# Kernel optimization log

Measured on AMD Instinct MI355X. Metric: run time of the kernel, lower is better.

Reference implementation:

```python
import jax, jax.numpy as jnp
import numpy as np

B, S, D, H, HD = 2, 4096, 768, 12, 64
W = 256           # one-sided window (attention_window=512)
C = S // W        # number of query chunks
NEG = -1e9


def _heads(x):
    # [B,S,D] -> [B,H,S,HD]
    return x.reshape(B, S, H, HD).transpose(0, 2, 1, 3)


def setup_inputs() -> dict:
    key = jax.random.key(0)
    ks = jax.random.split(key, 9)
    sc = 0.02
    w = lambda i: jax.random.normal(ks[i], (D, D), jnp.float32) * sc
    return {
        "hidden_states": jax.random.normal(ks[0], (B, S, D), jnp.float32),
        "Wq": w(1), "Wk": w(2), "Wv": w(3),
        "Wqg": w(4), "Wkg": w(5), "Wvg": w(6),
        "Wo": w(7),
        "attention_mask": jnp.ones((B, S), jnp.int32),
    }


def reference(hidden_states, Wq, Wk, Wv, Wqg, Wkg, Wvg, Wo, attention_mask):
    x = hidden_states
    scale = 1.0 / float(np.sqrt(HD))
    q = _heads(x @ Wq) * scale           # [B,H,S,HD]
    k = _heads(x @ Wk)
    v = _heads(x @ Wv)

    # ---- banded sliding-window attention (chunked, no [S,S] matrix) ----
    idx = jnp.arange(C)[:, None] * W + jnp.arange(3 * W)[None, :]   # [C,3W] into padded seq
    key_pos = idx - W                                               # absolute key position
    kp = jnp.pad(k, ((0, 0), (0, 0), (W, W), (0, 0)))
    vp = jnp.pad(v, ((0, 0), (0, 0), (W, W), (0, 0)))
    kc = kp[:, :, idx]                   # [B,H,C,3W,HD]
    vc = vp[:, :, idx]
    qc = q.reshape(B, H, C, W, HD)
    band = jnp.einsum('bhcqd,bhckd->bhcqk', qc, kc)  # [B,H,C,W,3W]

    qi = jnp.arange(W)[:, None]
    kj = jnp.arange(3 * W)[None, :]
    diag_ok = (kj >= qi) & (kj <= qi + 2 * W)              # |i-j| <= W
    valid = (key_pos >= 0) & (key_pos < S) & (key_pos != 0)  # in-range, dedupe global key 0
    mask = diag_ok[None, :, :] & valid[:, None, :]          # [C,W,3W]
    band = jnp.where(mask[None, None], band, NEG)

    # padding mask on keys
    m = jnp.where(attention_mask > 0, 0.0, NEG).astype(jnp.float32)  # [B,S]
    mp = jnp.pad(m, ((0, 0), (W, W)), constant_values=NEG)
    band = band + mp[:, idx][:, None, :, None, :]
    band = band.reshape(B, H, S, 3 * W)

    # every local query also attends to the global (CLS, pos 0) key
    gsc = jnp.einsum('bhsd,bhgd->bhsg', q, k[:, :, 0:1])   # [B,H,S,1]
    gsc = gsc + m[:, 0][:, None, None, None]

    scores = jnp.concatenate([gsc, band], axis=-1)          # [B,H,S,1+3W]
    probs = jax.nn.softmax(scores, axis=-1)
    pg = probs[..., :1]                                     # global-key prob
    pb = probs[..., 1:].reshape(B, H, C, W, 3 * W)
    out = jnp.einsum('bhcqk,bhckd->bhcqd', pb, vc).reshape(B, H, S, HD)
    out = out + pg * v[:, :, 0:1]

    # ---- global query (CLS) full attention with dedicated projections ----
    qg = _heads(x @ Wqg)[:, :, 0:1] * scale                 # [B,H,1,HD]
    kg = _heads(x @ Wkg)
    vg = _heads(x @ Wvg)
    gs = jnp.einsum('bhgd,bhsd->bhgs', qg, kg) + m[:, None, None, :]
    og = jnp.einsum('bhgs,bhsd->bhgd', jax.nn.softmax(gs, axis=-1), vg)
    out = out.at[:, :, 0:1].set(og)

    out = out.transpose(0, 2, 1, 3).reshape(B, S, D) @ Wo
    return out
```

## Files before the change

### kernel.cpp

```cpp
#include <hip/hip_runtime.h>

#define S_LEN 4096
#define NH 12
#define HDIM 64
#define DMODEL 768
#define NEGF -1.0e9f
#define TOK0_SPLITS 16

typedef __attribute__((ext_vector_type(8))) short bf16x8;
typedef __attribute__((ext_vector_type(4))) float f32x4;

__device__ __forceinline__ short f2b(float f) {
  union { float f; unsigned u; } v; v.f = f;
  unsigned r = v.u + 0x7fffu + ((v.u >> 16) & 1u);
  return (short)(r >> 16);
}
__device__ __forceinline__ float b2f(short s) {
  union { unsigned u; float f; } v; v.u = ((unsigned)(unsigned short)s) << 16;
  return v.f;
}

__global__ void k_conv_x(const float* __restrict__ x, short* __restrict__ xb, int n4) {
  int i = blockIdx.x * blockDim.x + threadIdx.x;
  if (i >= n4) return;
  float4 v = ((const float4*)x)[i];
  ((short4*)xb)[i] = make_short4(f2b(v.x), f2b(v.y), f2b(v.z), f2b(v.w));
}

__global__ void k_mv(const int* __restrict__ amask, float* __restrict__ mvb) {
  int b = blockIdx.y, s = blockIdx.x * 256 + threadIdx.x;
  mvb[b * S_LEN + s] = (s != 0 && amask[b * S_LEN + s] > 0) ? 0.f : NEGF;
}

__global__ void k_wt(const float* __restrict__ Wq, const float* __restrict__ Wk,
                     const float* __restrict__ Wv, const float* __restrict__ Wkg,
                     const float* __restrict__ Wvg, const float* __restrict__ Wo,
                     short* __restrict__ W5t, short* __restrict__ Wot) {
  __shared__ float tbuf[32][33];
  int z = blockIdx.z;
  const float* src; float scale = 1.f; short* dst;
  switch (z) {
    case 0: src = Wq;  scale = 0.125f * 1.44269504f; dst = W5t; break;
    case 1: src = Wk;  dst = W5t + 589824; break;
    case 2: src = Wv;  dst = W5t + 2 * 589824; break;
    case 3: src = Wkg; dst = W5t + 3 * 589824; break;
    case 4: src = Wvg; dst = W5t + 4 * 589824; break;
    default: src = Wo; dst = Wot; break;
  }
  int tx = threadIdx.x, ty = threadIdx.y;
  int kb = blockIdx.y * 32, nb = blockIdx.x * 32;
  for (int i = 0; i < 4; i++) tbuf[ty + 8 * i][tx] = src[(kb + ty + 8 * i) * 768 + nb + tx];
  __syncthreads();
  for (int i = 0; i < 4; i++)
    dst[(nb + ty + 8 * i) * 768 + kb + tx] = f2b(tbuf[tx][ty + 8 * i] * scale);
}

__global__ __launch_bounds__(256) void k_qg(const float* __restrict__ x,
                                            const float* __restrict__ Wqg,
                                            float* __restrict__ qg) {
  int h = blockIdx.x, b = blockIdx.y;
  int tid = threadIdx.x;
  int out = tid & 63, slice = tid >> 6;
  __shared__ float xr[768];
  __shared__ float ps[4][64];
  for (int i = tid; i < 768; i += 256) xr[i] = x[(long)b * S_LEN * 768 + i];
  __syncthreads();
  float a = 0.f;
  int n = h * 64 + out;
#pragma unroll 8
  for (int k = slice * 192; k < slice * 192 + 192; k++) a += xr[k] * Wqg[k * 768 + n];
  ps[slice][out] = a;
  __syncthreads();
  if (tid < 64)
    qg[b * 768 + h * 64 + tid] = (ps[0][tid] + ps[1][tid] + ps[2][tid] + ps[3][tid]) * 0.125f;
}

__global__ __launch_bounds__(256) void k_gemm(const short* __restrict__ A,
                                              const short* __restrict__ Bt, int K, int mode,
                                              short* __restrict__ qkv, float* __restrict__ outf) {
  __shared__ short Al[128 * 32];
  __shared__ short Bl[128 * 32];
  int bid = blockIdx.x;
  int xcd = bid & 7, ii = bid >> 3;
  int bm = xcd * 8 + (ii & 7), bn = ii >> 3;
  int tid = threadIdx.x;
  int bm0 = bm * 128, bn0 = bn * 128;
  int w = tid >> 6, lane = tid & 63, g = lane >> 4, r16 = lane & 15;
  int wr = (w >> 1) * 64, wc = (w & 1) * 64;
  f32x4 zero4 = {0.f, 0.f, 0.f, 0.f};
  f32x4 acc[4][4];
  for (int m = 0; m < 4; m++) for (int n = 0; n < 4; n++) acc[m][n] = zero4;
  int srow = w * 32 + (lane >> 2);
  int scol = (lane & 3) * 8;
  for (int kt = 0; kt < K; kt += 32) {
    for (int i = 0; i < 2; i++) {
      const short* ga = &A[(long)(bm0 + srow + i * 16) * K + kt + scol];
      const short* gb = &Bt[(long)(bn0 + srow + i * 16) * K + kt + scol];
      __builtin_amdgcn_global_load_lds(
          (const __attribute__((address_space(1))) void*)ga,
          (__attribute__((address_space(3))) void*)&Al[(w * 32 + i * 16) * 32], 16, 0, 0);
      __builtin_amdgcn_global_load_lds(
          (const __attribute__((address_space(1))) void*)gb,
          (__attribute__((address_space(3))) void*)&Bl[(w * 32 + i * 16) * 32], 16, 0, 0);
    }
    __syncthreads();
    bf16x8 af[4], bfv[4];
    for (int m = 0; m < 4; m++) af[m] = *(const bf16x8*)&Al[(wr + m * 16 + r16) * 32 + g * 8];
    for (int n = 0; n < 4; n++) bfv[n] = *(const bf16x8*)&Bl[(wc + n * 16 + r16) * 32 + g * 8];
    for (int m = 0; m < 4; m++)
      for (int n = 0; n < 4; n++)
        acc[m][n] = __builtin_amdgcn_mfma_f32_16x16x32_bf16(af[m], bfv[n], acc[m][n], 0, 0, 0);
    __syncthreads();
  }
  for (int m = 0; m < 4; m++)
    for (int n = 0; n < 4; n++)
      for (int reg = 0; reg < 4; reg++) {
        int row = bm0 + wr + m * 16 + g * 4 + reg;
        int col = bn0 + wc + n * 16 + r16;
        float val = acc[m][n][reg];
        if (mode == 0) {
          int proj = col / 768;
          int rem = col - proj * 768;
          int hh = rem >> 6, d = rem & 63;
          int bb = row >> 12, s = row & 4095;
          qkv[(long)proj * 6291456 + ((((long)bb * NH + hh) * S_LEN + s) << 6) + d] = f2b(val);
        } else {
          outf[(long)row * 768 + col] = val;
        }
      }
}

__global__ __launch_bounds__(256) void k_vt(const short* __restrict__ V, short* __restrict__ Vt) {
  __shared__ short buf[64][72];
  int st = blockIdx.x, bh = blockIdx.y;
  int tid = threadIdx.x;
  long base = (long)bh * S_LEN * HDIM;
  int s0 = st * 64;
  int r = tid >> 2, c = (tid & 3) * 16;
  *(int4*)&buf[r][c]     = *(const int4*)&V[base + (long)(s0 + r) * HDIM + c];
  *(int4*)&buf[r][c + 8] = *(const int4*)&V[base + (long)(s0 + r) * HDIM + c + 8];
  __syncthreads();
  int d = tid >> 2, sc = (tid & 3) * 16;
  short tmp[16];
#pragma unroll
  for (int j = 0; j < 16; j++) tmp[j] = buf[sc + j][d];
  long ob = base + (long)d * S_LEN + s0 + sc;
  *(int4*)&Vt[ob]     = *(const int4*)&tmp[0];
  *(int4*)&Vt[ob + 8] = *(const int4*)&tmp[8];
}

#define KVPAD 36
#define PSTRIDE 68

__device__ __forceinline__ void band_chunk(
    int ks0, int qrow0, int g, int r16,
    const bf16x8 (&qf)[2][2], const bf16x8 (&kf)[4][2], const bf16x8 (&vf)[4][2],
    const float (&mv)[4],
    float (&mstate)[2][4], float (&lstate)[2][4], f32x4 (&acc)[2][4],
    short* Plds) {
  int dlo = ks0 - qrow0;
  bool fullok = (dlo >= -224) && (dlo <= 192);
  for (int m = 0; m < 2; m++) {
    f32x4 s[4];
    f32x4 zero4 = {0.f, 0.f, 0.f, 0.f};
    for (int n = 0; n < 4; n++) {
      f32x4 z = __builtin_amdgcn_mfma_f32_16x16x32_bf16(qf[m][0], kf[n][0], zero4, 0, 0, 0);
      s[n] = __builtin_amdgcn_mfma_f32_16x16x32_bf16(qf[m][1], kf[n][1], z, 0, 0, 0);
    }
    float p[4][4], rmax[4];
    for (int reg = 0; reg < 4; reg++) rmax[reg] = NEGF;
    if (fullok) {
      for (int n = 0; n < 4; n++)
        for (int reg = 0; reg < 4; reg++) {
          float val = s[n][reg] + mv[n];
          p[n][reg] = val;
          rmax[reg] = fmaxf(rmax[reg], val);
        }
    } else {
      int qbase = qrow0 + m * 16 + g * 4;
      for (int n = 0; n < 4; n++) {
        int kpos = ks0 + n * 16 + r16;
        for (int reg = 0; reg < 4; reg++) {
          int qpos = qbase + reg;
          bool ok = (kpos >= qpos - 256) && (kpos <= qpos + 256);
          float val = ok ? (s[n][reg] + mv[n]) : NEGF;
          p[n][reg] = val;
          rmax[reg] = fmaxf(rmax[reg], val);
        }
      }
    }
    for (int reg = 0; reg < 4; reg++) {
      float r = rmax[reg];
      r = fmaxf(r, __shfl_xor(r, 1));
      r = fmaxf(r, __shfl_xor(r, 2));
      r = fmaxf(r, __shfl_xor(r, 4));
      r = fmaxf(r, __shfl_xor(r, 8));
      rmax[reg] = r;
    }
    bool over = false;
    for (int reg = 0; reg < 4; reg++) over = over || (rmax[reg] > mstate[m][reg] + 8.f);
    if (__any((int)over)) {
      float scal[4];
      for (int reg = 0; reg < 4; reg++) {
        float mn = fmaxf(mstate[m][reg], rmax[reg]);
        scal[reg] = __builtin_amdgcn_exp2f(mstate[m][reg] - mn);
        mstate[m][reg] = mn;
      }
      float rs[4] = {0.f, 0.f, 0.f, 0.f};
      for (int n = 0; n < 4; n++)
        for (int reg = 0; reg < 4; reg++) {
          float e = __builtin_amdgcn_exp2f(p[n][reg] - mstate[m][reg]);
          p[n][reg] = e;
          rs[reg] += e;
        }
      for (int reg = 0; reg < 4; reg++) {
        float r = rs[reg];
        r += __shfl_xor(r, 1);
        r += __shfl_xor(r, 2);
        r += __shfl_xor(r, 4);
        r += __shfl_xor(r, 8);
        lstate[m][reg] = lstate[m][reg] * scal[reg] + r;
      }
      for (int n = 0; n < 4; n++)
        for (int reg = 0; reg < 4; reg++) acc[m][n][reg] *= scal[reg];
    } else {
      float rs[4] = {0.f, 0.f, 0.f, 0.f};
      for (int n = 0; n < 4; n++)
        for (int reg = 0; reg < 4; reg++) {
          float e = __builtin_amdgcn_exp2f(p[n][reg] - mstate[m][reg]);
          p[n][reg] = e;
          rs[reg] += e;
        }
      for (int reg = 0; reg < 4; reg++) {
        float r = rs[reg];
        r += __shfl_xor(r, 1);
        r += __shfl_xor(r, 2);
        r += __shfl_xor(r, 4);
        r += __shfl_xor(r, 8);
        lstate[m][reg] += r;
      }
    }
    for (int n = 0; n < 4; n++)
      for (int reg = 0; reg < 4; reg++)
        Plds[(g * 4 + reg) * PSTRIDE + n * 16 + r16] = f2b(p[n][reg]);
    bf16x8 pa[2];
    for (int ks = 0; ks < 2; ks++)
      pa[ks] = *(const bf16x8*)&Plds[r16 * PSTRIDE + ks * 32 + g * 8];
    for (int n = 0; n < 4; n++)
      for (int ks = 0; ks < 2; ks++)
        acc[m][n] = __builtin_amdgcn_mfma_f32_16x16x32_bf16(pa[ks], vf[n][ks], acc[m][n], 0, 0, 0);
  }
}

__global__ __launch_bounds__(256, 2) void k_band(const short* __restrict__ Qb,
                                                 const short* __restrict__ Kb,
                                                 const short* __restrict__ Vb,
                                                 const short* __restrict__ Vtb,
                                                 const int* __restrict__ amask,
                                                 const float* __restrict__ mvb,
                                                 short* __restrict__ oattn) {
  int qtb = blockIdx.x, h = blockIdx.y, b = blockIdx.z;
  int tid = threadIdx.x, w = tid >> 6, lane = tid & 63, g = lane >> 4, r16 = lane & 15;
  long bhof = ((long)(b * NH + h)) * S_LEN * HDIM;
  __shared__ short Klds[2][2][64][KVPAD];
  __shared__ short Vlds[2][2][64][KVPAD];
  __shared__ short Plds[4][16 * PSTRIDE];
  int qb0 = qtb * 128;
  int qrow0 = qb0 + w * 32;

  bf16x8 qf[2][2];
  for (int m = 0; m < 2; m++)
    for (int ks = 0; ks < 2; ks++)
      qf[m][ks] = *(const bf16x8*)&Qb[bhof + (long)(qrow0 + m * 16 + r16) * HDIM + ks * 32 + g * 8];

  float mstate[2][4], lstate[2][4];
  f32x4 acc[2][4];
  {
    bf16x8 k0f[2];
    for (int ks = 0; ks < 2; ks++) k0f[ks] = *(const bf16x8*)&Kb[bhof + ks * 32 + g * 8];
    float part[2];
    for (int m = 0; m < 2; m++) {
      float p = 0.f;
      for (int ks = 0; ks < 2; ks++)
        for (int j = 0; j < 8; j++) p += b2f(qf[m][ks][j]) * b2f(k0f[ks][j]);
      p += __shfl_xor(p, 16);
      p += __shfl_xor(p, 32);
      part[m] = p;
    }
    float mask0 = (amask[b * S_LEN] > 0) ? 0.f : NEGF;
    float v0v[4];
    for (int n = 0; n < 4; n++) v0v[n] = b2f(Vb[bhof + n * 16 + r16]);
    for (int m = 0; m < 2; m++)
      for (int reg = 0; reg < 4; reg++) {
        mstate[m][reg] = __shfl(part[m], g * 4 + reg) + mask0;
        lstate[m][reg] = 1.f;
        for (int n = 0; n < 4; n++) acc[m][n][reg] = v0v[n];
      }
  }

  int c0 = (qb0 - 256) >> 6; if (c0 < 0) c0 = 0;
  int c1 = (qb0 + 127 + 256) >> 6; if (c1 > 63) c1 = 63;
  int wlo = (qrow0 - 256) >> 6;
  int whi = (qrow0 + 31 + 256) >> 6;

  int ss = tid >> 2, qq = tid & 3;
  int ksh = qq >> 1, qcol = (qq & 1) * 16;
  int4 rk0, rk1, rv0, rv1;
#define STAGE_LOAD(CI)                                                              \
  do {                                                                              \
    int _k = (CI) * 64;                                                             \
    const int4* gk = (const int4*)&Kb[bhof + (long)(_k + ss) * HDIM + qq * 16];     \
    rk0 = gk[0]; rk1 = gk[1];                                                       \
    const int4* gv = (const int4*)&Vtb[bhof + (long)ss * S_LEN + _k + qq * 16];     \
    rv0 = gv[0]; rv1 = gv[1];                                                       \
  } while (0)
#define STAGE_WRITE(BUF)                                                            \
  do {                                                                              \
    short* kd = &Klds[BUF][ksh][ss][qcol];                                          \
    *(int4*)kd = rk0; *(int4*)(kd + 8) = rk1;                                       \
    short* vd = &Vlds[BUF][ksh][ss][qcol];                                          \
    *(int4*)vd = rv0; *(int4*)(vd + 8) = rv1;                                       \
  } while (0)

  STAGE_LOAD(c0);
  STAGE_WRITE(0);
  __syncthreads();

  for (int ci = c0; ci <= c1; ci++) {
    int buf = (ci - c0) & 1;
    bool havenext = (ci + 1 <= c1);
    if (havenext) STAGE_LOAD(ci + 1);
    if (ci >= wlo && ci <= whi) {
      int ks0 = ci * 64;
      bf16x8 kf[4][2], vf[4][2];
      for (int n = 0; n < 4; n++)
        for (int ks = 0; ks < 2; ks++) {
          kf[n][ks] = *(const bf16x8*)&Klds[buf][ks][n * 16 + r16][g * 8];
          vf[n][ks] = *(const bf16x8*)&Vlds[buf][ks][n * 16 + r16][g * 8];
        }
      float mv[4];
      for (int n = 0; n < 4; n++) mv[n] = mvb[b * S_LEN + ks0 + n * 16 + r16];
      band_chunk(ks0, qrow0, g, r16, qf, kf, vf, mv, mstate, lstate, acc, &Plds[w][0]);
    }
    if (havenext) STAGE_WRITE(buf ^ 1);
    __syncthreads();
  }
#undef STAGE_LOAD
#undef STAGE_WRITE

  for (int m = 0; m < 2; m++)
    for (int n = 0; n < 4; n++)
      for (int reg = 0; reg < 4; reg++) {
        int token = qrow0 + m * 16 + g * 4 + reg;
        int col = h * 64 + n * 16 + r16;
        oattn[((long)b * S_LEN + token) * 768 + col] = f2b(acc[m][n][reg] / lstate[m][reg]);
      }
}

__global__ __launch_bounds__(256) void k_tok0_part(const float* __restrict__ qg,
                                                   const short* __restrict__ Kg,
                                                   const short* __restrict__ Vg,
                                                   const int* __restrict__ amask,
                                                   float* __restrict__ part) {
  int split = blockIdx.x, bhid = blockIdx.y;
  int b = bhid / NH, h = bhid % NH;
  long base = (long)bhid * S_LEN * HDIM;
  int tid = threadIdx.x, lane = tid & 63, w = tid >> 6;
  int s = split * 256 + tid;
  __shared__ float qgl[64];
  __shared__ float p_sh[256];
  __shared__ float red[4];
  __shared__ float psum[4][64];
  if (tid < 64) qgl[tid] = qg[b * 768 + h * 64 + tid];
  __syncthreads();
  float dot = 0.f;
  {
    const int4* kr = (const int4*)&Kg[base + (long)s * HDIM];
#pragma unroll
    for (int u = 0; u < 8; u++) {
      int4 pk = kr[u];
      const short* sp = (const short*)&pk;
      for (int j = 0; j < 8; j++) dot += qgl[u * 8 + j] * b2f(sp[j]);
    }
    dot += (amask[b * S_LEN + s] > 0) ? 0.f : NEGF;
  }
  float mx = dot;
  for (int o = 32; o; o >>= 1) mx = fmaxf(mx, __shfl_xor(mx, o));
  if (lane == 0) red[w] = mx;
  __syncthreads();
  mx = fmaxf(fmaxf(red[0], red[1]), fmaxf(red[2], red[3]));
  float e = __expf(dot - mx);
  p_sh[tid] = e;
  float sum = e;
  for (int o = 32; o; o >>= 1) sum += __shfl_xor(sum, o);
  __syncthreads();
  if (lane == 0) red[w] = sum;
  __syncthreads();
  sum = red[0] + red[1] + red[2] + red[3];
  int d = tid & 63, grp = tid >> 6;
  float a = 0.f;
  long vb = base + (long)(split * 256 + grp * 64) * HDIM + d;
#pragma unroll 8
  for (int j = 0; j < 64; j++) a += p_sh[grp * 64 + j] * b2f(Vg[vb + (long)j * HDIM]);
  psum[grp][d] = a;
  __syncthreads();
  float* dst = &part[((long)bhid * TOK0_SPLITS + split) * 66];
  if (tid == 0) { dst[0] = mx; dst[1] = sum; }
  if (tid < 64) dst[2 + tid] = psum[0][tid] + psum[1][tid] + psum[2][tid] + psum[3][tid];
}

__global__ void k_tok0_comb(const float* __restrict__ part, short* __restrict__ oattn) {
  int bhid = blockIdx.x, d = threadIdx.x;
  int b = bhid / NH, h = bhid % NH;
  const float* p0 = &part[(long)bhid * TOK0_SPLITS * 66];
  float M = NEGF;
  for (int i = 0; i < TOK0_SPLITS; i++) M = fmaxf(M, p0[i * 66]);
  float L = 0.f, a = 0.f;
  for (int i = 0; i < TOK0_SPLITS; i++) {
    float sc = __expf(p0[i * 66] - M);
    L += sc * p0[i * 66 + 1];
    a += sc * p0[i * 66 + 2 + d];
  }
  oattn[((long)b * S_LEN) * 768 + h * 64 + d] = f2b(a / L);
}

extern "C" void kernel_launch(void* const* d_in, const int* in_sizes, int n_in,
                              void* d_out, int out_size, void* d_ws, size_t ws_size,
                              hipStream_t stream) {
  (void)in_sizes; (void)n_in; (void)out_size; (void)ws_size;
  const float* x   = (const float*)d_in[0];
  const float* Wq  = (const float*)d_in[1];
  const float* Wk  = (const float*)d_in[2];
  const float* Wv  = (const float*)d_in[3];
  const float* Wqg = (const float*)d_in[4];
  const float* Wkg = (const float*)d_in[5];
  const float* Wvg = (const float*)d_in[6];
  const float* Wo  = (const float*)d_in[7];
  const int* amask = (const int*)d_in[8];
  char* ws = (char*)d_ws;
  short* xb    = (short*)(ws);
  short* Vt    = (short*)(ws);
  short* W5t   = (short*)(ws + 12582912);
  short* Wot   = (short*)(ws + 18481152);
  short* qkv   = (short*)(ws + 19660800);
  short* oattn = (short*)(ws + 82575360);
  float* qgbuf = (float*)(ws + 95158272);
  float* partb = (float*)(ws + 95164416);
  float* mvb   = (float*)(ws + 95265792);
  float* outf  = (float*)d_out;

  k_conv_x<<<6144, 256, 0, stream>>>(x, xb, 1572864);
  k_mv<<<dim3(16, 2), 256, 0, stream>>>(amask, mvb);
  k_wt<<<dim3(24, 24, 6), dim3(32, 8), 0, stream>>>(Wq, Wk, Wv, Wkg, Wvg, Wo, W5t, Wot);
  k_qg<<<dim3(12, 2), 256, 0, stream>>>(x, Wqg, qgbuf);
  k_gemm<<<1920, 256, 0, stream>>>(xb, W5t, 768, 0, qkv, nullptr);
  const short* Qb = qkv;
  const short* Kb = qkv + 6291456;
  const short* Vb = qkv + 2 * 6291456;
  const short* Kg = qkv + 3 * 6291456;
  const short* Vg = qkv + 4 * 6291456;
  k_vt<<<dim3(64, 24), 256, 0, stream>>>(Vb, Vt);
  k_band<<<dim3(32, 12, 2), 256, 0, stream>>>(Qb, Kb, Vb, Vt, amask, mvb, oattn);
  k_tok0_part<<<dim3(TOK0_SPLITS, 24), 256, 0, stream>>>(qgbuf, Kg, Vg, amask, partb);
  k_tok0_comb<<<24, 64, 0, stream>>>(partb, oattn);
  k_gemm<<<384, 256, 0, stream>>>(oattn, Wot, 768, 1, nullptr, outf);
}
```

Before: 227.9 us.

## Fuse preprocessing kernels into one launch and double-buffer GEMM LDS tiles

Four small preprocessing kernels (x to bf16 conversion, weight transpose-convert, mask vector, CLS query projection) are merged into one launch, with block ranges dispatching to each task, to cut launch overhead and gaps between kernels. The projection GEMM gets two LDS buffers so the global-to-LDS load of the next K tile is issued before the MFMAs on the current tile. This doubles the GEMM's LDS use, which may reduce occupancy. The merged kernel sizes its shared memory for the largest branch.

```diff
diff --git a/kernel.cpp b/kernel.cpp
--- a/kernel.cpp
+++ b/kernel.cpp
@@ -20,66 +20,73 @@
   return v.f;
 }
 
-__global__ void k_conv_x(const float* __restrict__ x, short* __restrict__ xb, int n4) {
-  int i = blockIdx.x * blockDim.x + threadIdx.x;
-  if (i >= n4) return;
-  float4 v = ((const float4*)x)[i];
-  ((short4*)xb)[i] = make_short4(f2b(v.x), f2b(v.y), f2b(v.z), f2b(v.w));
-}
-
-__global__ void k_mv(const int* __restrict__ amask, float* __restrict__ mvb) {
-  int b = blockIdx.y, s = blockIdx.x * 256 + threadIdx.x;
-  mvb[b * S_LEN + s] = (s != 0 && amask[b * S_LEN + s] > 0) ? 0.f : NEGF;
-}
-
-__global__ void k_wt(const float* __restrict__ Wq, const float* __restrict__ Wk,
-                     const float* __restrict__ Wv, const float* __restrict__ Wkg,
-                     const float* __restrict__ Wvg, const float* __restrict__ Wo,
-                     short* __restrict__ W5t, short* __restrict__ Wot) {
-  __shared__ float tbuf[32][33];
-  int z = blockIdx.z;
-  const float* src; float scale = 1.f; short* dst;
-  switch (z) {
-    case 0: src = Wq;  scale = 0.125f * 1.44269504f; dst = W5t; break;
-    case 1: src = Wk;  dst = W5t + 589824; break;
-    case 2: src = Wv;  dst = W5t + 2 * 589824; break;
-    case 3: src = Wkg; dst = W5t + 3 * 589824; break;
-    case 4: src = Wvg; dst = W5t + 4 * 589824; break;
-    default: src = Wo; dst = Wot; break;
-  }
-  int tx = threadIdx.x, ty = threadIdx.y;
-  int kb = blockIdx.y * 32, nb = blockIdx.x * 32;
-  for (int i = 0; i < 4; i++) tbuf[ty + 8 * i][tx] = src[(kb + ty + 8 * i) * 768 + nb + tx];
-  __syncthreads();
-  for (int i = 0; i < 4; i++)
-    dst[(nb + ty + 8 * i) * 768 + kb + tx] = f2b(tbuf[tx][ty + 8 * i] * scale);
-}
-
-__global__ __launch_bounds__(256) void k_qg(const float* __restrict__ x,
-                                            const float* __restrict__ Wqg,
-                                            float* __restrict__ qg) {
-  int h = blockIdx.x, b = blockIdx.y;
-  int tid = threadIdx.x;
-  int out = tid & 63, slice = tid >> 6;
-  __shared__ float xr[768];
-  __shared__ float ps[4][64];
-  for (int i = tid; i < 768; i += 256) xr[i] = x[(long)b * S_LEN * 768 + i];
-  __syncthreads();
-  float a = 0.f;
-  int n = h * 64 + out;
+__global__ __launch_bounds__(256) void k_pre(const float* __restrict__ x,
+                                             const float* __restrict__ Wq,
+                                             const float* __restrict__ Wk,
+                                             const float* __restrict__ Wv,
+                                             const float* __restrict__ Wkg,
+                                             const float* __restrict__ Wvg,
+                                             const float* __restrict__ Wo,
+                                             const float* __restrict__ Wqg,
+                                             const int* __restrict__ amask,
+                                             short* __restrict__ xb,
+                                             short* __restrict__ W5t,
+                                             short* __restrict__ Wot,
+                                             float* __restrict__ qg,
+                                             float* __restrict__ mvb) {
+  __shared__ float smem[1056];
+  int bid = blockIdx.x, tid = threadIdx.x;
+  if (bid < 6144) {
+    int i = bid * 256 + tid;
+    float4 v = ((const float4*)x)[i];
+    ((short4*)xb)[i] = make_short4(f2b(v.x), f2b(v.y), f2b(v.z), f2b(v.w));
+  } else if (bid < 9600) {
+    int zb = bid - 6144;
+    int z = zb / 576, rem = zb - z * 576;
+    int by = rem / 24, bx = rem - by * 24;
+    const float* src; float scale = 1.f; short* dst;
+    switch (z) {
+      case 0: src = Wq;  scale = 0.125f * 1.44269504f; dst = W5t; break;
+      case 1: src = Wk;  dst = W5t + 589824; break;
+      case 2: src = Wv;  dst = W5t + 2 * 589824; break;
+      case 3: src = Wkg; dst = W5t + 3 * 589824; break;
+      case 4: src = Wvg; dst = W5t + 4 * 589824; break;
+      default: src = Wo; dst = Wot; break;
+    }
+    int tx = tid & 31, ty = tid >> 5;
+    int kb = by * 32, nb = bx * 32;
+    for (int i = 0; i < 4; i++) smem[(ty + 8 * i) * 33 + tx] = src[(kb + ty + 8 * i) * 768 + nb + tx];
+    __syncthreads();
+    for (int i = 0; i < 4; i++)
+      dst[(nb + ty + 8 * i) * 768 + kb + tx] = f2b(smem[tx * 33 + ty + 8 * i] * scale);
+  } else if (bid < 9632) {
+    int zb = bid - 9600;
+    int b = zb >> 4, s = (zb & 15) * 256 + tid;
+    mvb[b * S_LEN + s] = (s != 0 && amask[b * S_LEN + s] > 0) ? 0.f : NEGF;
+  } else {
+    int zb = bid - 9632;
+    int h = zb % 12, b = zb / 12;
+    int out = tid & 63, slice = tid >> 6;
+    float* xr = smem;
+    float* ps = smem + 768;
+    for (int i = tid; i < 768; i += 256) xr[i] = x[(long)b * S_LEN * 768 + i];
+    __syncthreads();
+    float a = 0.f;
+    int n = h * 64 + out;
 #pragma unroll 8
-  for (int k = slice * 192; k < slice * 192 + 192; k++) a += xr[k] * Wqg[k * 768 + n];
-  ps[slice][out] = a;
-  __syncthreads();
-  if (tid < 64)
-    qg[b * 768 + h * 64 + tid] = (ps[0][tid] + ps[1][tid] + ps[2][tid] + ps[3][tid]) * 0.125f;
+    for (int k = slice * 192; k < slice * 192 + 192; k++) a += xr[k] * Wqg[k * 768 + n];
+    ps[slice * 64 + out] = a;
+    __syncthreads();
+    if (tid < 64)
+      qg[b * 768 + h * 64 + tid] = (ps[tid] + ps[64 + tid] + ps[128 + tid] + ps[192 + tid]) * 0.125f;
+  }
 }
 
 __global__ __launch_bounds__(256) void k_gemm(const short* __restrict__ A,
                                               const short* __restrict__ Bt, int K, int mode,
                                               short* __restrict__ qkv, float* __restrict__ outf) {
-  __shared__ short Al[128 * 32];
-  __shared__ short Bl[128 * 32];
+  __shared__ short Al[2][128 * 32];
+  __shared__ short Bl[2][128 * 32];
   int bid = blockIdx.x;
   int xcd = bid & 7, ii = bid >> 3;
   int bm = xcd * 8 + (ii & 7), bn = ii >> 3;
@@ -92,26 +99,37 @@
   for (int m = 0; m < 4; m++) for (int n = 0; n < 4; n++) acc[m][n] = zero4;
   int srow = w * 32 + (lane >> 2);
   int scol = (lane & 3) * 8;
-  for (int kt = 0; kt < K; kt += 32) {
-    for (int i = 0; i < 2; i++) {
-      const short* ga = &A[(long)(bm0 + srow + i * 16) * K + kt + scol];
-      const short* gb = &Bt[(long)(bn0 + srow + i * 16) * K + kt + scol];
-      __builtin_amdgcn_global_load_lds(
-          (const __attribute__((address_space(1))) void*)ga,
-          (__attribute__((address_space(3))) void*)&Al[(w * 32 + i * 16) * 32], 16, 0, 0);
-      __builtin_amdgcn_global_load_lds(
-          (const __attribute__((address_space(1))) void*)gb,
-          (__attribute__((address_space(3))) void*)&Bl[(w * 32 + i * 16) * 32], 16, 0, 0);
-    }
-    __syncthreads();
+#define G_STAGE(BUF, KT)                                                              \
+  do {                                                                                \
+    for (int i = 0; i < 2; i++) {                                                     \
+      const short* ga = &A[(long)(bm0 + srow + i * 16) * K + (KT) + scol];            \
+      const short* gb = &Bt[(long)(bn0 + srow + i * 16) * K + (KT) + scol];           \
+      __builtin_amdgcn_global_load_lds(                                               \
+          (const __attribute__((address_space(1))) void*)ga,                          \
+          (__attribute__((address_space(3))) void*)&Al[BUF][(w * 32 + i * 16) * 32],  \
+          16, 0, 0);                                                                  \
+      __builtin_amdgcn_global_load_lds(                                               \
+          (const __attribute__((address_space(1))) void*)gb,                          \
+          (__attribute__((address_space(3))) void*)&Bl[BUF][(w * 32 + i * 16) * 32],  \
+          16, 0, 0);                                                                  \
+    }                                                                                 \
+  } while (0)
+  int nt = K >> 5;
+  G_STAGE(0, 0);
+  __syncthreads();
+  int cur = 0;
+  for (int t = 0; t < nt; t++) {
+    if (t + 1 < nt) G_STAGE(cur ^ 1, (t + 1) * 32);
     bf16x8 af[4], bfv[4];
-    for (int m = 0; m < 4; m++) af[m] = *(const bf16x8*)&Al[(wr + m * 16 + r16) * 32 + g * 8];
-    for (int n = 0; n < 4; n++) bfv[n] = *(const bf16x8*)&Bl[(wc + n * 16 + r16) * 32 + g * 8];
+    for (int m = 0; m < 4; m++) af[m] = *(const bf16x8*)&Al[cur][(wr + m * 16 + r16) * 32 + g * 8];
+    for (int n = 0; n < 4; n++) bfv[n] = *(const bf16x8*)&Bl[cur][(wc + n * 16 + r16) * 32 + g * 8];
     for (int m = 0; m < 4; m++)
       for (int n = 0; n < 4; n++)
         acc[m][n] = __builtin_amdgcn_mfma_f32_16x16x32_bf16(af[m], bfv[n], acc[m][n], 0, 0, 0);
     __syncthreads();
-  }
+    cur ^= 1;
+  }
+#undef G_STAGE
   for (int m = 0; m < 4; m++)
     for (int n = 0; n < 4; n++)
       for (int reg = 0; reg < 4; reg++) {
@@ -449,10 +467,8 @@
   float* mvb   = (float*)(ws + 95265792);
   float* outf  = (float*)d_out;
 
-  k_conv_x<<<6144, 256, 0, stream>>>(x, xb, 1572864);
-  k_mv<<<dim3(16, 2), 256, 0, stream>>>(amask, mvb);
-  k_wt<<<dim3(24, 24, 6), dim3(32, 8), 0, stream>>>(Wq, Wk, Wv, Wkg, Wvg, Wo, W5t, Wot);
-  k_qg<<<dim3(12, 2), 256, 0, stream>>>(x, Wqg, qgbuf);
+  k_pre<<<9656, 256, 0, stream>>>(x, Wq, Wk, Wv, Wkg, Wvg, Wo, Wqg, amask,
+                                  xb, W5t, Wot, qgbuf, mvb);
   k_gemm<<<1920, 256, 0, stream>>>(xb, W5t, 768, 0, qkv, nullptr);
   const short* Qb = qkv;
   const short* Kb = qkv + 6291456;
```

New measurement: 215.2 us. 1.06x faster.
